# Kernel tuning notes

Hardware: AMD Instinct MI355X
Metric: run time of the kernel (lower is better)

Reference implementation:

```python
import jax, jax.numpy as jnp
import numpy as np

B, N, P, M = 64, 64, 512, 512  # batch, num objects, max pairs, message_size


def setup_inputs() -> dict:
    key = jax.random.key(0)
    k1, k2, k3, k4 = jax.random.split(key, 4)
    obj_ft = jax.random.normal(k1, (B, N, M), dtype=jnp.float32)
    node_embeddings = jax.random.normal(k2, (B, N, M), dtype=jnp.float32)
    edge_embeddings = jax.random.normal(k3, (B, N, N, M), dtype=jnp.float32)
    pairs = jax.random.randint(k4, (B, P, 2), 0, N, dtype=jnp.int64)
    return {
        "obj_ft": obj_ft,
        "node_embeddings": node_embeddings,
        "edge_embeddings": edge_embeddings,
        "pairs": pairs,
    }


def reference(obj_ft, node_embeddings, edge_embeddings, pairs):
    """Vectorized make_classifier_inputs.

    Output layout (last dim = 3M):
      [:2M] = mean(concat(node_emb[i0], node_emb[i1]), concat(obj_ft[i0], obj_ft[i1]))
      [2M:] = mean(edge_emb[i0,i1], edge_emb[i1,i0])
    """
    i0 = pairs[..., 0]  # [B, P]
    i1 = pairs[..., 1]  # [B, P]
    b_idx = jnp.arange(pairs.shape[0])[:, None]  # [B, 1] broadcasts against [B, P]

    # edge part: mean of the two directed edge embeddings -> [B, P, M]
    e01 = edge_embeddings[b_idx, i0, i1]
    e10 = edge_embeddings[b_idx, i1, i0]
    temp_e = 0.5 * (e01 + e10)

    # node part: mean of concat'd GNN embeddings and concat'd resized object features
    n_cat = jnp.concatenate([node_embeddings[b_idx, i0], node_embeddings[b_idx, i1]], axis=-1)  # [B,P,2M]
    o_cat = jnp.concatenate([obj_ft[b_idx, i0], obj_ft[b_idx, i1]], axis=-1)  # [B,P,2M]
    temp_n = 0.5 * (n_cat + o_cat)

    return jnp.concatenate([temp_n, temp_e], axis=-1)  # [B, P, 3M]
```

## Files before the change

kernel.cpp:

```cpp
#include <hip/hip_runtime.h>

#define B_ 64
#define N_ 64
#define P_ 512
#define M_ 512

__global__ __launch_bounds__(128) void ooi_gather_kernel(
    const float* __restrict__ obj_ft,
    const float* __restrict__ node_emb,
    const float* __restrict__ edge_emb,
    const int*   __restrict__ pairs,
    float* __restrict__ out)
{
    const int bp = blockIdx.x;
    const int b  = bp >> 9;
    const int t  = threadIdx.x;

    const int i0 = pairs[2 * bp + 0];
    const int i1 = pairs[2 * bp + 1];

    const size_t bn0 = (size_t)(b * N_ + i0);
    const size_t bn1 = (size_t)(b * N_ + i1);

    const float4* n0  = (const float4*)(node_emb + bn0 * M_);
    const float4* n1  = (const float4*)(node_emb + bn1 * M_);
    const float4* o0  = (const float4*)(obj_ft   + bn0 * M_);
    const float4* o1  = (const float4*)(obj_ft   + bn1 * M_);
    const float4* e01 = (const float4*)(edge_emb + (bn0 * N_ + i1) * (size_t)M_);
    const float4* e10 = (const float4*)(edge_emb + (bn1 * N_ + i0) * (size_t)M_);

    float4* outp = (float4*)(out + (size_t)bp * (3 * M_));

    {
        float4 a = n0[t], c = o0[t], r;
        r.x = 0.5f * (a.x + c.x);
        r.y = 0.5f * (a.y + c.y);
        r.z = 0.5f * (a.z + c.z);
        r.w = 0.5f * (a.w + c.w);
        outp[t] = r;
    }
    {
        float4 a = n1[t], c = o1[t], r;
        r.x = 0.5f * (a.x + c.x);
        r.y = 0.5f * (a.y + c.y);
        r.z = 0.5f * (a.z + c.z);
        r.w = 0.5f * (a.w + c.w);
        outp[128 + t] = r;
    }
    {
        float4 a = e01[t], c = e10[t], r;
        r.x = 0.5f * (a.x + c.x);
        r.y = 0.5f * (a.y + c.y);
        r.z = 0.5f * (a.z + c.z);
        r.w = 0.5f * (a.w + c.w);
        outp[256 + t] = r;
    }
}

extern "C" void kernel_launch(void* const* d_in, const int* in_sizes, int n_in,
                              void* d_out, int out_size, void* d_ws, size_t ws_size,
                              hipStream_t stream) {
    const float* obj_ft   = (const float*)d_in[0];
    const float* node_emb = (const float*)d_in[1];
    const float* edge_emb = (const float*)d_in[2];
    const int*   pairs    = (const int*)d_in[3];
    float* out = (float*)d_out;

    dim3 grid(B_ * P_);
    dim3 block(128);
    ooi_gather_kernel<<<grid, block, 0, stream>>>(obj_ft, node_emb, edge_emb,
                                                  pairs, out);
}
```

Measured before the change: 665.6 us.

## Process eight pairs per block with XCD-grouped remap and nontemporal stores

Each 256-thread block now handles eight pairs, two halves of the block each doing four, and issues all of a pair's row loads together to raise memory parallelism. Block indices are remapped so consecutive pair groups (same batch) land on the same XCD, improving L2 reuse of node, object and edge rows. Output writes use nontemporal stores to avoid polluting cache with streamed results. Fewer blocks may reduce latency hiding if occupancy drops.

```diff
diff --git a/kernel.cpp b/kernel.cpp
--- a/kernel.cpp
+++ b/kernel.cpp
@@ -5,55 +5,60 @@
 #define P_ 512
 #define M_ 512
 
-__global__ __launch_bounds__(128) void ooi_gather_kernel(
+#define PPB  8
+#define NBLK (B_ * P_ / PPB)
+#define NXCD 8
+
+typedef float f4 __attribute__((ext_vector_type(4)));
+
+__global__ __launch_bounds__(256) void ooi_gather_kernel(
     const float* __restrict__ obj_ft,
     const float* __restrict__ node_emb,
     const float* __restrict__ edge_emb,
     const int*   __restrict__ pairs,
     float* __restrict__ out)
 {
-    const int bp = blockIdx.x;
-    const int b  = bp >> 9;
-    const int t  = threadIdx.x;
+    const int L  = blockIdx.x;
+    const int vb = (L & (NXCD - 1)) * (NBLK / NXCD) + (L >> 3);
 
-    const int i0 = pairs[2 * bp + 0];
-    const int i1 = pairs[2 * bp + 1];
+    const int half = threadIdx.x >> 7;
+    const int t    = threadIdx.x & 127;
 
-    const size_t bn0 = (size_t)(b * N_ + i0);
-    const size_t bn1 = (size_t)(b * N_ + i1);
+    const int pair_base = vb * PPB;
+    const int b         = pair_base >> 9;
 
-    const float4* n0  = (const float4*)(node_emb + bn0 * M_);
-    const float4* n1  = (const float4*)(node_emb + bn1 * M_);
-    const float4* o0  = (const float4*)(obj_ft   + bn0 * M_);
-    const float4* o1  = (const float4*)(obj_ft   + bn1 * M_);
-    const float4* e01 = (const float4*)(edge_emb + (bn0 * N_ + i1) * (size_t)M_);
-    const float4* e10 = (const float4*)(edge_emb + (bn1 * N_ + i0) * (size_t)M_);
+    const int2* pairs2 = (const int2*)pairs;
+    int2 pr[PPB / 2];
+    #pragma unroll
+    for (int k = 0; k < PPB / 2; ++k)
+        pr[k] = pairs2[pair_base + 2 * k + half];
 
-    float4* outp = (float4*)(out + (size_t)bp * (3 * M_));
+    const float* nb = node_emb + (size_t)b * (N_ * M_);
+    const float* ob = obj_ft   + (size_t)b * (N_ * M_);
+    const float* eb = edge_emb + (size_t)b * ((size_t)N_ * N_ * M_);
 
-    {
-        float4 a = n0[t], c = o0[t], r;
-        r.x = 0.5f * (a.x + c.x);
-        r.y = 0.5f * (a.y + c.y);
-        r.z = 0.5f * (a.z + c.z);
-        r.w = 0.5f * (a.w + c.w);
-        outp[t] = r;
-    }
-    {
-        float4 a = n1[t], c = o1[t], r;
-        r.x = 0.5f * (a.x + c.x);
-        r.y = 0.5f * (a.y + c.y);
-        r.z = 0.5f * (a.z + c.z);
-        r.w = 0.5f * (a.w + c.w);
-        outp[128 + t] = r;
-    }
-    {
-        float4 a = e01[t], c = e10[t], r;
-        r.x = 0.5f * (a.x + c.x);
-        r.y = 0.5f * (a.y + c.y);
-        r.z = 0.5f * (a.z + c.z);
-        r.w = 0.5f * (a.w + c.w);
-        outp[256 + t] = r;
+    #pragma unroll
+    for (int k = 0; k < PPB / 2; ++k) {
+        const int p  = pair_base + 2 * k + half;
+        const int i0 = pr[k].x;
+        const int i1 = pr[k].y;
+
+        const f4* n0  = (const f4*)(nb + (size_t)i0 * M_);
+        const f4* n1  = (const f4*)(nb + (size_t)i1 * M_);
+        const f4* o0  = (const f4*)(ob + (size_t)i0 * M_);
+        const f4* o1  = (const f4*)(ob + (size_t)i1 * M_);
+        const f4* e01 = (const f4*)(eb + ((size_t)(i0 * N_ + i1)) * M_);
+        const f4* e10 = (const f4*)(eb + ((size_t)(i1 * N_ + i0)) * M_);
+
+        f4* outp = (f4*)(out + (size_t)p * (3 * M_));
+
+        f4 a0 = n0[t],  c0 = o0[t];
+        f4 a1 = n1[t],  c1 = o1[t];
+        f4 a2 = e01[t], c2 = e10[t];
+
+        __builtin_nontemporal_store(0.5f * (a0 + c0), outp + t);
+        __builtin_nontemporal_store(0.5f * (a1 + c1), outp + 128 + t);
+        __builtin_nontemporal_store(0.5f * (a2 + c2), outp + 256 + t);
     }
 }
 
@@ -66,8 +71,8 @@
     const int*   pairs    = (const int*)d_in[3];
     float* out = (float*)d_out;
 
-    dim3 grid(B_ * P_);
-    dim3 block(128);
+    dim3 grid(NBLK);
+    dim3 block(256);
     ooi_gather_kernel<<<grid, block, 0, stream>>>(obj_ft, node_emb, edge_emb,
                                                   pairs, out);
 }
```

New measurement: 674.3 us. About the same (+1.3%).

## Precompute per-node average into workspace, then gather pairs with nontemporal stores

Applied to the files above, without the earlier changes.

Adds a pre-pass kernel that computes 0.5*(node_emb+obj_ft) once per node into the workspace. The pair kernel then gathers two precomputed rows plus the two edge rows, so each pair does four row loads instead of six. It also uses 384 threads per block and nontemporal loads and stores for the streaming edge input and the output. The catch is an extra kernel launch and a full pass over the node tensors. If the workspace is too small, it falls back to a fused kernel with nontemporal stores.

```diff
diff --git a/kernel.cpp b/kernel.cpp
--- a/kernel.cpp
+++ b/kernel.cpp
@@ -5,7 +5,55 @@
 #define P_ 512
 #define M_ 512
 
-__global__ __launch_bounds__(128) void ooi_gather_kernel(
+typedef float f4 __attribute__((ext_vector_type(4)));
+
+#define S_BYTES ((size_t)B_ * N_ * M_ * sizeof(float))
+
+__global__ __launch_bounds__(256) void precompute_s_kernel(
+    const float* __restrict__ obj_ft,
+    const float* __restrict__ node_emb,
+    float* __restrict__ s)
+{
+    const int idx = blockIdx.x * 256 + threadIdx.x;
+    const f4* n = (const f4*)node_emb;
+    const f4* o = (const f4*)obj_ft;
+    ((f4*)s)[idx] = 0.5f * (n[idx] + o[idx]);
+}
+
+__global__ __launch_bounds__(384) void gather_pairs_kernel(
+    const float* __restrict__ s,
+    const float* __restrict__ edge_emb,
+    const int*   __restrict__ pairs,
+    float* __restrict__ out)
+{
+    const int bp  = blockIdx.x;
+    const int b   = bp >> 9;
+    const int tid = threadIdx.x;
+
+    const int i0 = pairs[2 * bp + 0];
+    const int i1 = pairs[2 * bp + 1];
+
+    f4* outp = (f4*)(out + (size_t)bp * (3 * M_));
+
+    if (tid < 256) {
+        const int which = tid >> 7;
+        const int t     = tid & 127;
+        const int idx   = which ? i1 : i0;
+        const f4* srow  = (const f4*)(s + (size_t)(b * N_ + idx) * M_);
+        __builtin_nontemporal_store(srow[t], outp + (which << 7) + t);
+    } else {
+        const int t = tid - 256;
+        const size_t bn0 = (size_t)(b * N_ + i0);
+        const size_t bn1 = (size_t)(b * N_ + i1);
+        const f4* e01 = (const f4*)(edge_emb + (bn0 * N_ + i1) * (size_t)M_);
+        const f4* e10 = (const f4*)(edge_emb + (bn1 * N_ + i0) * (size_t)M_);
+        f4 a = __builtin_nontemporal_load(e01 + t);
+        f4 c = __builtin_nontemporal_load(e10 + t);
+        __builtin_nontemporal_store(0.5f * (a + c), outp + 256 + t);
+    }
+}
+
+__global__ __launch_bounds__(128) void gather_fused_kernel(
     const float* __restrict__ obj_ft,
     const float* __restrict__ node_emb,
     const float* __restrict__ edge_emb,
@@ -22,39 +70,18 @@
     const size_t bn0 = (size_t)(b * N_ + i0);
     const size_t bn1 = (size_t)(b * N_ + i1);
 
-    const float4* n0  = (const float4*)(node_emb + bn0 * M_);
-    const float4* n1  = (const float4*)(node_emb + bn1 * M_);
-    const float4* o0  = (const float4*)(obj_ft   + bn0 * M_);
-    const float4* o1  = (const float4*)(obj_ft   + bn1 * M_);
-    const float4* e01 = (const float4*)(edge_emb + (bn0 * N_ + i1) * (size_t)M_);
-    const float4* e10 = (const float4*)(edge_emb + (bn1 * N_ + i0) * (size_t)M_);
+    const f4* n0  = (const f4*)(node_emb + bn0 * M_);
+    const f4* n1  = (const f4*)(node_emb + bn1 * M_);
+    const f4* o0  = (const f4*)(obj_ft   + bn0 * M_);
+    const f4* o1  = (const f4*)(obj_ft   + bn1 * M_);
+    const f4* e01 = (const f4*)(edge_emb + (bn0 * N_ + i1) * (size_t)M_);
+    const f4* e10 = (const f4*)(edge_emb + (bn1 * N_ + i0) * (size_t)M_);
 
-    float4* outp = (float4*)(out + (size_t)bp * (3 * M_));
+    f4* outp = (f4*)(out + (size_t)bp * (3 * M_));
 
-    {
-        float4 a = n0[t], c = o0[t], r;
-        r.x = 0.5f * (a.x + c.x);
-        r.y = 0.5f * (a.y + c.y);
-        r.z = 0.5f * (a.z + c.z);
-        r.w = 0.5f * (a.w + c.w);
-        outp[t] = r;
-    }
-    {
-        float4 a = n1[t], c = o1[t], r;
-        r.x = 0.5f * (a.x + c.x);
-        r.y = 0.5f * (a.y + c.y);
-        r.z = 0.5f * (a.z + c.z);
-        r.w = 0.5f * (a.w + c.w);
-        outp[128 + t] = r;
-    }
-    {
-        float4 a = e01[t], c = e10[t], r;
-        r.x = 0.5f * (a.x + c.x);
-        r.y = 0.5f * (a.y + c.y);
-        r.z = 0.5f * (a.z + c.z);
-        r.w = 0.5f * (a.w + c.w);
-        outp[256 + t] = r;
-    }
+    __builtin_nontemporal_store(0.5f * (n0[t] + o0[t]), outp + t);
+    __builtin_nontemporal_store(0.5f * (n1[t] + o1[t]), outp + 128 + t);
+    __builtin_nontemporal_store(0.5f * (e01[t] + e10[t]), outp + 256 + t);
 }
 
 extern "C" void kernel_launch(void* const* d_in, const int* in_sizes, int n_in,
@@ -66,8 +93,14 @@
     const int*   pairs    = (const int*)d_in[3];
     float* out = (float*)d_out;
 
-    dim3 grid(B_ * P_);
-    dim3 block(128);
-    ooi_gather_kernel<<<grid, block, 0, stream>>>(obj_ft, node_emb, edge_emb,
-                                                  pairs, out);
+    if (d_ws != nullptr && ws_size >= S_BYTES) {
+        float* s = (float*)d_ws;
+        precompute_s_kernel<<<dim3(B_ * N_ * M_ / 4 / 256), dim3(256), 0, stream>>>(
+            obj_ft, node_emb, s);
+        gather_pairs_kernel<<<dim3(B_ * P_), dim3(384), 0, stream>>>(
+            s, edge_emb, pairs, out);
+    } else {
+        gather_fused_kernel<<<dim3(B_ * P_), dim3(128), 0, stream>>>(
+            obj_ft, node_emb, edge_emb, pairs, out);
+    }
 }
```

After: 667.0 us. Within noise of the previous version (+0.2%).
